# Optimization experiments

Measured on AMD Instinct MI355X. Metric: run time of the kernel, lower is better.

Reference implementation:

```python
import jax, jax.numpy as jnp
import numpy as np

# --- constants from init_kwargs / module defaults ---
H, W, C = 720, 1280, 2
T_EVT, T_PROP = 10, 10
T_TOTAL = T_EVT + T_PROP          # 20 temporal steps (10 event + 10 propagation)
TAU, THR0 = 10.0, 1.0             # LIF time constant, base threshold
ALPHA, TARGET_RATE = 0.1, 0.1     # PENT adaptation
THR_MIN, THR_MAX = 0.1, 10.0
N_EVENTS = 4_000_000


def setup_inputs() -> dict:
    key = jax.random.key(0)
    k1, k2, k3, k4 = jax.random.split(key, 4)
    x = jax.random.randint(k1, (N_EVENTS,), 0, W, dtype=jnp.int32)
    y = jax.random.randint(k2, (N_EVENTS,), 0, H, dtype=jnp.int32)
    p = jax.random.randint(k3, (N_EVENTS,), 0, 2, dtype=jnp.int32)
    t = jax.random.uniform(k4, (N_EVENTS,), dtype=jnp.float32)
    return {"x": x, "y": y, "p": p, "t": t}


def _build_buffer(x, y, p, t):
    # TemporalBuffer.forward: bin events into first T_EVT steps, rest are zeros.
    tmin, tmax = t.min(), t.max()
    denom = jnp.where(tmax > tmin, tmax - tmin, jnp.float32(1.0))
    t_norm = jnp.where(tmax > tmin, (t - tmin) / denom * (T_EVT - 1e-6), 0.0)
    t_idx = jnp.clip(t_norm.astype(jnp.int32), 0, T_EVT - 1)
    xi = jnp.clip(x, 0, W - 1)
    yi = jnp.clip(y, 0, H - 1)
    c_idx = p  # p in {0,1} -> channel index directly (p.min() >= 0 branch)
    buf = jnp.zeros((T_TOTAL, C, H, W), jnp.float32)
    return buf.at[t_idx, c_idx, yi, xi].add(1.0)


def reference(x, y, p, t):
    buffer = _build_buffer(x, y, p, t)  # (T, C, H, W)
    decay = jnp.float32(np.exp(-1.0 / TAU))

    def step(carry, frame):
        mem, thr = carry
        # LIFBuffer: decay + accumulate
        mem = mem * decay + frame
        spk = (mem >= thr).astype(jnp.float32)
        mem = mem - spk * thr  # soft ('subtract') reset
        # AdaptiveThreshold (PENT): homeostatic rate-based adaptation
        rate = spk.mean()
        thr = jnp.clip(thr + ALPHA * (rate - TARGET_RATE), THR_MIN, THR_MAX)
        return (mem, thr), spk

    mem0 = jnp.zeros((C, H, W), jnp.float32)
    (_, _), spikes = jax.lax.scan(step, (mem0, jnp.float32(THR0)), buffer)
    return spikes  # (T, C, H, W) binary spike activity maps
```

## Files before the change

kernel.cpp:

```cpp
#include <hip/hip_runtime.h>
#include <cstddef>

#define HH 720
#define WW 1280
#define FRAME 1843200
#define FRAME4 460800
#define T_EVT 10
#define T_TOTAL 20
#define ARRIVE64 (1ULL << 32)

#define ONBLK 256
#define ONTHR 1024
#define ONWPB 16
#define ONT (ONBLK * ONTHR)

#define SBLK 1024
#define STHR 256
#define SWPB 4
#define PIXB 1800
#define NGROUP4 450
#define HIST_W 9000
#define RBLK 512
#define RTHR 1024
#define NBUCKET 1024
#define EPT 8
#define MAXM (EPT * RTHR)
#define MMBLK 128
#define MMTHR 1024

#define MAT_OFF   0u
#define MMX_OFF   (512u * 1024u * 4u)
#define KEY_OFF   (MMX_OFF + 4096u)
#define WS_NEED(chunk) ((size_t)KEY_OFF + 2ull * RBLK * (size_t)(chunk) + 256ull)

__device__ unsigned g_minkey;
__device__ unsigned g_maxkey;
__device__ unsigned long long g_grp[T_TOTAL][16][16];
__device__ unsigned long long g_top[T_TOTAL][16];
__device__ unsigned g_rel[T_TOTAL][32];
__device__ unsigned long long g_n1[T_TOTAL][64][16];
__device__ unsigned long long g_n2[T_TOTAL][4][16];
__device__ unsigned long long g_n3[T_TOTAL][16];
__device__ unsigned g_relg[T_TOTAL][64][32];

__device__ __forceinline__ unsigned f2key(float f) {
    unsigned b = __float_as_uint(f);
    return b ^ ((unsigned)(((int)b) >> 31) | 0x80000000u);
}
__device__ __forceinline__ float key2f(unsigned k) {
    unsigned b = (k & 0x80000000u) ? (k ^ 0x80000000u) : ~k;
    return __uint_as_float(b);
}

__device__ __forceinline__ int event_bin_t(float tv, float tmin, float tmax) {
#pragma clang fp contract(off)
    float tn;
    if (tmax > tmin) tn = (tv - tmin) / (tmax - tmin) * (float)(10.0 - 1e-6);
    else tn = 0.0f;
    int ti = (int)tn;
    return ti < 0 ? 0 : (ti > T_EVT - 1 ? T_EVT - 1 : ti);
}
__device__ __forceinline__ int event_pixel(int xi, int yi, int ci) {
    xi = xi < 0 ? 0 : (xi > WW - 1 ? WW - 1 : xi);
    yi = yi < 0 ? 0 : (yi > HH - 1 ? HH - 1 : yi);
    return ci * (HH * WW) + yi * WW + xi;
}

__global__ void init_kernel() {
    const int gtid = blockIdx.x * blockDim.x + threadIdx.x;
    const int gs = gridDim.x * blockDim.x;
    if (gtid == 0) { g_minkey = 0xFFFFFFFFu; g_maxkey = 0u; }
    unsigned long long* a = &g_grp[0][0][0];
    for (int i = gtid; i < T_TOTAL * 16 * 16; i += gs) a[i] = 0ull;
    unsigned long long* b = &g_top[0][0];
    for (int i = gtid; i < T_TOTAL * 16; i += gs) b[i] = 0ull;
    unsigned* c = &g_rel[0][0];
    for (int i = gtid; i < T_TOTAL * 32; i += gs) c[i] = 0u;
}

__device__ __forceinline__ void minmax_body(const float* __restrict__ t, int n,
                                            int gtid, int gstride) {
    unsigned mn = 0xFFFFFFFFu, mx = 0u;
    const int n4 = n >> 2;
    const float4* t4 = (const float4*)t;
    for (int i = gtid; i < n4; i += gstride) {
        float4 tv = t4[i];
        unsigned k0 = f2key(tv.x), k1 = f2key(tv.y);
        unsigned k2 = f2key(tv.z), k3 = f2key(tv.w);
        unsigned a = k0 < k1 ? k0 : k1, b = k2 < k3 ? k2 : k3;
        unsigned c = a < b ? a : b;
        mn = mn < c ? mn : c;
        a = k0 > k1 ? k0 : k1; b = k2 > k3 ? k2 : k3;
        c = a > b ? a : b;
        mx = mx > c ? mx : c;
    }
    for (int i = (n4 << 2) + gtid; i < n; i += gstride) {
        unsigned k = f2key(t[i]);
        mn = mn < k ? mn : k;
        mx = mx > k ? mx : k;
    }
    for (int off = 32; off > 0; off >>= 1) {
        unsigned omn = (unsigned)__shfl_down((int)mn, off, 64);
        unsigned omx = (unsigned)__shfl_down((int)mx, off, 64);
        mn = mn < omn ? mn : omn;
        mx = mx > omx ? mx : omx;
    }
    __shared__ unsigned smn[16], smx[16];
    int lane = threadIdx.x & 63, wv = threadIdx.x >> 6;
    if (lane == 0) { smn[wv] = mn; smx[wv] = mx; }
    __syncthreads();
    if (threadIdx.x == 0) {
        int nw = blockDim.x >> 6;
        for (int i = 1; i < nw; ++i) {
            mn = mn < smn[i] ? mn : smn[i];
            mx = mx > smx[i] ? mx : smx[i];
        }
        atomicMin(&g_minkey, mn);
        atomicMax(&g_maxkey, mx);
    }
}

__global__ void minmax_zero_kernel(const float* __restrict__ t, int n,
                                   uint4* __restrict__ hist16v) {
    const int gtid = blockIdx.x * blockDim.x + threadIdx.x;
    const int gstride = gridDim.x * blockDim.x;
    const uint4 z = make_uint4(0u, 0u, 0u, 0u);
    const int nz = T_EVT * FRAME / 8;
    for (int i = gtid; i < nz; i += gstride) hist16v[i] = z;
    minmax_body(t, n, gtid, gstride);
}

__global__ __launch_bounds__(MMTHR) void minmax_ws_kernel(
        const float* __restrict__ t, int n, unsigned* __restrict__ mmx) {
    const int gtid = blockIdx.x * blockDim.x + threadIdx.x;
    const int gstride = gridDim.x * blockDim.x;
    unsigned mx = 0u, imn = 0u;
    const int n4 = n >> 2;
    const float4* t4 = (const float4*)t;
    for (int i = gtid; i < n4; i += gstride) {
        float4 tv = t4[i];
        unsigned k0 = f2key(tv.x), k1 = f2key(tv.y);
        unsigned k2 = f2key(tv.z), k3 = f2key(tv.w);
        unsigned a = k0 > k1 ? k0 : k1, b = k2 > k3 ? k2 : k3;
        unsigned c = a > b ? a : b;
        mx = mx > c ? mx : c;
        unsigned i0 = ~k0, i1 = ~k1, i2 = ~k2, i3 = ~k3;
        a = i0 > i1 ? i0 : i1; b = i2 > i3 ? i2 : i3;
        c = a > b ? a : b;
        imn = imn > c ? imn : c;
    }
    for (int i = (n4 << 2) + gtid; i < n; i += gstride) {
        unsigned k = f2key(t[i]);
        mx = mx > k ? mx : k;
        unsigned ik = ~k;
        imn = imn > ik ? imn : ik;
    }
    for (int off = 32; off > 0; off >>= 1) {
        unsigned omx = (unsigned)__shfl_down((int)mx, off, 64);
        unsigned oim = (unsigned)__shfl_down((int)imn, off, 64);
        mx = mx > omx ? mx : omx;
        imn = imn > oim ? imn : oim;
    }
    __shared__ unsigned smx[MMTHR / 64], sim[MMTHR / 64];
    const int lane = threadIdx.x & 63, wv = threadIdx.x >> 6;
    if (lane == 0) { smx[wv] = mx; sim[wv] = imn; }
    __syncthreads();
    if (threadIdx.x == 0) {
#pragma unroll
        for (int i = 1; i < MMTHR / 64; ++i) {
            mx = mx > smx[i] ? mx : smx[i];
            imn = imn > sim[i] ? imn : sim[i];
        }
        atomicMax(&mmx[0], mx);
        atomicMax(&mmx[32], imn);
    }
}

__global__ __launch_bounds__(RTHR) void passAB_kernel(
        const int* __restrict__ x, const int* __restrict__ y,
        const int* __restrict__ p, const float* __restrict__ t,
        const unsigned* __restrict__ mmx,
        unsigned* __restrict__ mat, unsigned short* __restrict__ seg, int n) {
    __shared__ unsigned cnt[NBUCKET];
    __shared__ unsigned wt2[RTHR / 64];
    __shared__ unsigned short sorted[MAXM];
    const int bid = blockIdx.x;
    const int j = threadIdx.x;
    const int lane = j & 63, wv = j >> 6;
    const int gtid = bid * RTHR + j;
    const int gs = RBLK * RTHR;
    {
        unsigned long long* z1 = &g_n1[0][0][0];
        for (int i = gtid; i < T_TOTAL * 64 * 16; i += gs) z1[i] = 0ull;
        unsigned long long* z2 = &g_n2[0][0][0];
        for (int i = gtid; i < T_TOTAL * 4 * 16; i += gs) z2[i] = 0ull;
        unsigned long long* z3 = &g_n3[0][0];
        for (int i = gtid; i < T_TOTAL * 16; i += gs) z3[i] = 0ull;
        unsigned* z4 = &g_relg[0][0][0];
        for (int i = gtid; i < T_TOTAL * 64 * 32; i += gs) z4[i] = 0u;
    }
    cnt[j] = 0u;
    __syncthreads();
    const float tmax = key2f(mmx[0]);
    const float tmin = key2f(~mmx[32]);
    const int chunk = (((n + RBLK - 1) / RBLK) + 3) & ~3;
    const int s0 = bid * chunk;
    const int s1 = min(n, s0 + chunk);
    const int m = s1 - s0;

    unsigned rec[EPT];
#pragma unroll
    for (int k = 0; k < EPT / 4; ++k) {
        const int ibase = s0 + ((k * RTHR + j) << 2);
#pragma unroll
        for (int e = 0; e < 4; ++e) rec[k * 4 + e] = 0xFFFFFFFFu;
        if (ibase + 4 <= s1) {
            int4 xv = *(const int4*)(x + ibase);
            int4 yv = *(const int4*)(y + ibase);
            int4 pv = *(const int4*)(p + ibase);
            float4 tv = *(const float4*)(t + ibase);
            int pxs[4] = { event_pixel(xv.x, yv.x, pv.x),
                           event_pixel(xv.y, yv.y, pv.y),
                           event_pixel(xv.z, yv.z, pv.z),
                           event_pixel(xv.w, yv.w, pv.w) };
            float ts[4] = { tv.x, tv.y, tv.z, tv.w };
#pragma unroll
            for (int e = 0; e < 4; ++e) {
                int pix = pxs[e];
                int ti = event_bin_t(ts[e], tmin, tmax);
                int bkt = pix / PIXB;
                int lb = ti * PIXB + (pix - bkt * PIXB);
                rec[k * 4 + e] = ((unsigned)bkt << 16) | (unsigned)lb;
                atomicAdd(&cnt[bkt], 1u);
            }
        } else if (ibase < s1) {
            for (int e = 0; e < 4; ++e) {
                int i = ibase + e;
                if (i < s1) {
                    int pix = event_pixel(x[i], y[i], p[i]);
                    int ti = event_bin_t(t[i], tmin, tmax);
                    int bkt = pix / PIXB;
                    int lb = ti * PIXB + (pix - bkt * PIXB);
                    rec[k * 4 + e] = ((unsigned)bkt << 16) | (unsigned)lb;
                    atomicAdd(&cnt[bkt], 1u);
                }
            }
        }
    }
    __syncthreads();
    {
        unsigned v = cnt[j];
        unsigned incl = v;
        for (int off = 1; off < 64; off <<= 1) {
            unsigned o = (unsigned)__shfl_up((int)incl, off, 64);
            if (lane >= off) incl += o;
        }
        if (lane == 63) wt2[wv] = incl;
        __syncthreads();
        if (j == 0) {
            unsigned run = 0;
#pragma unroll
            for (int k = 0; k < RTHR / 64; ++k) { unsigned tmp = wt2[k]; wt2[k] = run; run += tmp; }
        }
        __syncthreads();
        unsigned ex = incl - v + wt2[wv];
        mat[bid * NBUCKET + j] = (ex << 16) | v;
        cnt[j] = ex;
    }
    __syncthreads();
#pragma unroll
    for (int k = 0; k < EPT; ++k) {
        unsigned r0 = rec[k];
        if (r0 != 0xFFFFFFFFu) {
            unsigned bkt = r0 >> 16;
            unsigned r = atomicAdd(&cnt[bkt], 1u);
            sorted[r] = (unsigned short)(r0 & 0xFFFFu);
        }
    }
    __syncthreads();
    unsigned short* segb = seg + (size_t)bid * (size_t)chunk;
    for (int i = j; i < m; i += RTHR) segb[i] = sorted[i];
}

__global__ __launch_bounds__(STHR, 4) void scan_new(float* __restrict__ out,
                                                    const unsigned short* __restrict__ seg,
                                                    const unsigned* __restrict__ mat,
                                                    int n) {
#pragma clang fp contract(off)
    const float decay = (float)0.9048374180359595;
    const int tid = threadIdx.x;
    const int lane = tid & 63;
    const int b = blockIdx.x;
    const int pix0 = b * PIXB;

    __shared__ alignas(16) unsigned lds_hist[HIST_W];
    __shared__ unsigned runw[RBLK];
    __shared__ unsigned lds_arr[T_TOTAL];
    __shared__ unsigned lds_tot[T_TOTAL];

    for (int i = tid; i < HIST_W; i += STHR) lds_hist[i] = 0u;
    for (int r = tid; r < RBLK; r += STHR) runw[r] = mat[r * NBUCKET + b];
    if (tid < T_TOTAL) { lds_arr[tid] = 0u; lds_tot[tid] = 0u; }
    __syncthreads();

    {
        const int chunk = (((n + RBLK - 1) / RBLK) + 3) & ~3;
        for (int r = tid; r < RBLK; r += STHR) {
            unsigned w = runw[r];
            unsigned c = w & 0xFFFFu;
            const unsigned short* sp = seg + (size_t)r * (size_t)chunk + (w >> 16);
            for (unsigned k = 0; k < c; ++k) {
                unsigned lb = sp[k];
                atomicAdd(&lds_hist[lb >> 1], 1u << ((lb & 1u) << 4));
            }
        }
    }
    __syncthreads();

    const bool has1 = tid < (NGROUP4 - STHR);
    float4 mem0 = make_float4(0.f, 0.f, 0.f, 0.f);
    float4 mem1 = make_float4(0.f, 0.f, 0.f, 0.f);
    float thr = 1.0f;

    float4 f0, f1;
    {
        uint2 w01 = *(const uint2*)&lds_hist[tid << 1];
        f0 = make_float4((float)(w01.x & 0xFFFFu), (float)(w01.x >> 16),
                         (float)(w01.y & 0xFFFFu), (float)(w01.y >> 16));
        if (has1) {
            uint2 v = *(const uint2*)&lds_hist[(tid + STHR) << 1];
            f1 = make_float4((float)(v.x & 0xFFFFu), (float)(v.x >> 16),
                             (float)(v.y & 0xFFFFu), (float)(v.y >> 16));
        } else f1 = make_float4(0.f, 0.f, 0.f, 0.f);
    }

    for (int s = 0;; ++s) {
        float* ob = out + (size_t)s * FRAME + pix0;
        int cnt = 0;

        {
            float4 m, spk;
            m.x = mem0.x + f0.x;
            m.y = mem0.y + f0.y;
            m.z = mem0.z + f0.z;
            m.w = mem0.w + f0.w;
            spk.x = (m.x >= thr) ? 1.0f : 0.0f;
            spk.y = (m.y >= thr) ? 1.0f : 0.0f;
            spk.z = (m.z >= thr) ? 1.0f : 0.0f;
            spk.w = (m.w >= thr) ? 1.0f : 0.0f;
            ((float4*)ob)[tid] = spk;
            mem0.x = m.x - spk.x * thr;
            mem0.y = m.y - spk.y * thr;
            mem0.z = m.z - spk.z * thr;
            mem0.w = m.w - spk.w * thr;
            cnt += (int)spk.x + (int)spk.y + (int)spk.z + (int)spk.w;
        }
        if (has1) {
            int g = tid + STHR;
            float4 m, spk;
            m.x = mem1.x + f1.x;
            m.y = mem1.y + f1.y;
            m.z = mem1.z + f1.z;
            m.w = mem1.w + f1.w;
            spk.x = (m.x >= thr) ? 1.0f : 0.0f;
            spk.y = (m.y >= thr) ? 1.0f : 0.0f;
            spk.z = (m.z >= thr) ? 1.0f : 0.0f;
            spk.w = (m.w >= thr) ? 1.0f : 0.0f;
            ((float4*)ob)[g] = spk;
            mem1.x = m.x - spk.x * thr;
            mem1.y = m.y - spk.y * thr;
            mem1.z = m.z - spk.z * thr;
            mem1.w = m.w - spk.w * thr;
            cnt += (int)spk.x + (int)spk.y + (int)spk.z + (int)spk.w;
        }

        if (s == T_TOTAL - 1) break;

        for (int off = 32; off > 0; off >>= 1) cnt += __shfl_down(cnt, off, 64);

        bool last = false;
        const int g1 = b >> 4;
        if (lane == 0) {
            unsigned old = __hip_atomic_fetch_add(&lds_arr[s],
                               (unsigned)cnt + (1u << 16),
                               __ATOMIC_RELAXED, __HIP_MEMORY_SCOPE_WORKGROUP);
            if ((old >> 16) == SWPB - 1) {
                last = true;
                unsigned bc = (old + (unsigned)cnt) & 0xFFFFu;
                unsigned long long a1 = __hip_atomic_fetch_add(
                    &g_n1[s][g1][0], (unsigned long long)bc + ARRIVE64,
                    __ATOMIC_RELAXED, __HIP_MEMORY_SCOPE_AGENT);
                if ((unsigned)(a1 >> 32) == 15u) {
                    unsigned c1 = (unsigned)a1 + bc;
                    const int g2 = g1 >> 4;
                    unsigned long long a2 = __hip_atomic_fetch_add(
                        &g_n2[s][g2][0], (unsigned long long)c1 + ARRIVE64,
                        __ATOMIC_RELAXED, __HIP_MEMORY_SCOPE_AGENT);
                    if ((unsigned)(a2 >> 32) == 15u) {
                        unsigned c2 = (unsigned)a2 + c1;
                        unsigned long long a3 = __hip_atomic_fetch_add(
                            &g_n3[s][0], (unsigned long long)c2 + ARRIVE64,
                            __ATOMIC_RELAXED, __HIP_MEMORY_SCOPE_AGENT);
                        if ((unsigned)(a3 >> 32) == 3u) {
                            unsigned tot = (unsigned)a3 + c2;
                            for (int g = 0; g < 64; ++g)
                                __hip_atomic_store(&g_relg[s][g][0], tot + 1u,
                                    __ATOMIC_RELAXED, __HIP_MEMORY_SCOPE_AGENT);
                        }
                    }
                }
            }
        }

        {
            const int sn = s + 1;
            if (sn < T_EVT) {
                uint2 w01 = *(const uint2*)&lds_hist[sn * 900 + (tid << 1)];
                f0 = make_float4((float)(w01.x & 0xFFFFu), (float)(w01.x >> 16),
                                 (float)(w01.y & 0xFFFFu), (float)(w01.y >> 16));
                if (has1) {
                    uint2 v = *(const uint2*)&lds_hist[sn * 900 + ((tid + STHR) << 1)];
                    f1 = make_float4((float)(v.x & 0xFFFFu), (float)(v.x >> 16),
                                     (float)(v.y & 0xFFFFu), (float)(v.y >> 16));
                }
            } else {
                f0 = make_float4(0.f, 0.f, 0.f, 0.f);
                f1 = make_float4(0.f, 0.f, 0.f, 0.f);
            }
            mem0.x = mem0.x * decay; mem0.y = mem0.y * decay;
            mem0.z = mem0.z * decay; mem0.w = mem0.w * decay;
            mem1.x = mem1.x * decay; mem1.y = mem1.y * decay;
            mem1.z = mem1.z * decay; mem1.w = mem1.w * decay;
        }
        __builtin_amdgcn_sched_barrier(0);

        unsigned total = 0u;
        if (lane == 0) {
            unsigned f;
            if (last) {
                do {
                    __builtin_amdgcn_s_sleep(1);
                    f = __hip_atomic_load(&g_relg[s][g1][0], __ATOMIC_RELAXED,
                                          __HIP_MEMORY_SCOPE_AGENT);
                } while (f == 0u);
                total = f - 1u;
                __hip_atomic_store(&lds_tot[s], f,
                                   __ATOMIC_RELAXED, __HIP_MEMORY_SCOPE_WORKGROUP);
            } else {
                unsigned f2;
                do {
                    __builtin_amdgcn_s_sleep(1);
                    f2 = __hip_atomic_load(&lds_tot[s], __ATOMIC_RELAXED,
                                           __HIP_MEMORY_SCOPE_WORKGROUP);
                } while (f2 == 0u);
                total = f2 - 1u;
            }
        }
        total = (unsigned)__shfl((int)total, 0, 64);
        float rate = (float)total / 1843200.0f;
        thr = thr + 0.1f * (rate - 0.1f);
        thr = fminf(fmaxf(thr, 0.1f), 10.0f);
    }
}

__global__ void scatter_kernel(const int* __restrict__ x, const int* __restrict__ y,
                               const int* __restrict__ p, const float* __restrict__ t,
                               unsigned* __restrict__ hist32, int n) {
    int i = blockIdx.x * blockDim.x + threadIdx.x;
    if (i >= n) return;
    float tmin = key2f(g_minkey);
    float tmax = key2f(g_maxkey);
    int ti = event_bin_t(t[i], tmin, tmax);
    int pix = event_pixel(x[i], y[i], p[i]);
    size_t bidx = (size_t)ti * FRAME + pix;
    atomicAdd(hist32 + (bidx >> 1), 1u << ((bidx & 1) << 4));
}

__global__ __launch_bounds__(ONTHR) void scan_old(float* __restrict__ out) {
#pragma clang fp contract(off)
    const float decay = (float)0.9048374180359595;
    const int gtid = blockIdx.x * ONTHR + threadIdx.x;
    const int lane = threadIdx.x & 63;
    const uint2 uz2 = make_uint2(0u, 0u);
    float4 mem0 = make_float4(0.f, 0.f, 0.f, 0.f);
    float4 mem1 = make_float4(0.f, 0.f, 0.f, 0.f);
    const bool has1 = (gtid + ONT) < FRAME4;
    float thr = 1.0f;
    const uint2* hist2 = (const uint2*)(out + (size_t)T_EVT * FRAME);
    __shared__ unsigned lds_arr[T_TOTAL];
    __shared__ unsigned lds_tot[T_TOTAL];
    if (threadIdx.x < T_TOTAL) { lds_arr[threadIdx.x] = 0u; lds_tot[threadIdx.x] = 0u; }
    __syncthreads();
    uint2 u0 = hist2[gtid];
    uint2 u1 = has1 ? hist2[gtid + ONT] : uz2;
    for (int s = 0; s < T_TOTAL; ++s) {
        float4* o4 = (float4*)(out + (size_t)s * FRAME);
        int cnt = 0;
        {
            float4 m, spk;
            m.x = mem0.x * decay; m.x = m.x + (float)(u0.x & 0xFFFFu);
            m.y = mem0.y * decay; m.y = m.y + (float)(u0.x >> 16);
            m.z = mem0.z * decay; m.z = m.z + (float)(u0.y & 0xFFFFu);
            m.w = mem0.w * decay; m.w = m.w + (float)(u0.y >> 16);
            spk.x = (m.x >= thr) ? 1.0f : 0.0f;
            spk.y = (m.y >= thr) ? 1.0f : 0.0f;
            spk.z = (m.z >= thr) ? 1.0f : 0.0f;
            spk.w = (m.w >= thr) ? 1.0f : 0.0f;
            o4[gtid] = spk;
            mem0.x = m.x - spk.x * thr; mem0.y = m.y - spk.y * thr;
            mem0.z = m.z - spk.z * thr; mem0.w = m.w - spk.w * thr;
            cnt += (int)spk.x + (int)spk.y + (int)spk.z + (int)spk.w;
        }
        if (has1) {
            float4 m, spk;
            m.x = mem1.x * decay; m.x = m.x + (float)(u1.x & 0xFFFFu);
            m.y = mem1.y * decay; m.y = m.y + (float)(u1.x >> 16);
            m.z = mem1.z * decay; m.z = m.z + (float)(u1.y & 0xFFFFu);
            m.w = mem1.w * decay; m.w = m.w + (float)(u1.y >> 16);
            spk.x = (m.x >= thr) ? 1.0f : 0.0f;
            spk.y = (m.y >= thr) ? 1.0f : 0.0f;
            spk.z = (m.z >= thr) ? 1.0f : 0.0f;
            spk.w = (m.w >= thr) ? 1.0f : 0.0f;
            o4[gtid + ONT] = spk;
            mem1.x = m.x - spk.x * thr; mem1.y = m.y - spk.y * thr;
            mem1.z = m.z - spk.z * thr; mem1.w = m.w - spk.w * thr;
            cnt += (int)spk.x + (int)spk.y + (int)spk.z + (int)spk.w;
        }
        if (s + 1 < T_EVT) {
            const uint2* hn = hist2 + (size_t)(s + 1) * FRAME4;
            u0 = hn[gtid];
            u1 = has1 ? hn[gtid + ONT] : uz2;
        } else { u0 = uz2; u1 = uz2; }
        if (s == T_TOTAL - 1) break;
        for (int off = 32; off > 0; off >>= 1) cnt += __shfl_down(cnt, off, 64);
        unsigned total = 0u;
        if (lane == 0) {
            unsigned old = __hip_atomic_fetch_add(&lds_arr[s],
                               (unsigned)cnt + (1u << 16),
                               __ATOMIC_RELAXED, __HIP_MEMORY_SCOPE_WORKGROUP);
            if ((old >> 16) == ONWPB - 1) {
                unsigned bc = (old + (unsigned)cnt) & 0xFFFFu;
                const int gid = blockIdx.x >> 4;
                unsigned long long gold = __hip_atomic_fetch_add(
                    &g_grp[s][gid][0], (unsigned long long)bc + ARRIVE64,
                    __ATOMIC_RELAXED, __HIP_MEMORY_SCOPE_AGENT);
                if ((unsigned)(gold >> 32) == 15u) {
                    unsigned gc = (unsigned)gold + bc;
                    unsigned long long told = __hip_atomic_fetch_add(
                        &g_top[s][0], (unsigned long long)gc + ARRIVE64,
                        __ATOMIC_RELAXED, __HIP_MEMORY_SCOPE_AGENT);
                    if ((unsigned)(told >> 32) == 15u) {
                        unsigned tot = (unsigned)told + gc;
                        __hip_atomic_store(&g_rel[s][0], tot + 1u,
                                           __ATOMIC_RELAXED, __HIP_MEMORY_SCOPE_AGENT);
                    }
                }
                unsigned f;
                do {
                    __builtin_amdgcn_s_sleep(1);
                    f = __hip_atomic_load(&g_rel[s][0], __ATOMIC_RELAXED,
                                          __HIP_MEMORY_SCOPE_AGENT);
                } while (f == 0u);
                total = f - 1u;
                __hip_atomic_store(&lds_tot[s], f,
                                   __ATOMIC_RELAXED, __HIP_MEMORY_SCOPE_WORKGROUP);
            } else {
                unsigned f;
                do {
                    __builtin_amdgcn_s_sleep(1);
                    f = __hip_atomic_load(&lds_tot[s], __ATOMIC_RELAXED,
                                          __HIP_MEMORY_SCOPE_WORKGROUP);
                } while (f == 0u);
                total = f - 1u;
            }
        }
        total = (unsigned)__shfl((int)total, 0, 64);
        float rate = (float)total / 1843200.0f;
        thr = thr + 0.1f * (rate - 0.1f);
        thr = fminf(fmaxf(thr, 0.1f), 10.0f);
    }
}

extern "C" void kernel_launch(void* const* d_in, const int* in_sizes, int n_in,
                              void* d_out, int out_size, void* d_ws, size_t ws_size,
                              hipStream_t stream) {
    const int*   x = (const int*)d_in[0];
    const int*   y = (const int*)d_in[1];
    const int*   p = (const int*)d_in[2];
    const float* t = (const float*)d_in[3];
    float* out = (float*)d_out;
    const int n = in_sizes[0];

    const int chunk = (((n + RBLK - 1) / RBLK) + 3) & ~3;
    if (d_ws != nullptr && ws_size >= WS_NEED(chunk) && chunk <= MAXM && n >= 4) {
        unsigned* mat = (unsigned*)((char*)d_ws + MAT_OFF);
        unsigned* mmx = (unsigned*)((char*)d_ws + MMX_OFF);
        unsigned short* seg = (unsigned short*)((char*)d_ws + KEY_OFF);

        hipMemsetAsync(mmx, 0, 256, stream);
        minmax_ws_kernel<<<MMBLK, MMTHR, 0, stream>>>(t, n, mmx);
        passAB_kernel<<<RBLK, RTHR, 0, stream>>>(x, y, p, t, mmx, mat, seg, n);

        dim3 g(SBLK), b(STHR);
        void* args[] = { (void*)&out, (void*)&seg, (void*)&mat, (void*)&n };
        hipLaunchCooperativeKernel((void*)scan_new, g, b, args, 0, stream);
    } else {
        init_kernel<<<64, 256, 0, stream>>>();
        unsigned* hist32 = (unsigned*)(out + (size_t)T_EVT * FRAME);
        minmax_zero_kernel<<<1024, 256, 0, stream>>>(t, n, (uint4*)hist32);
        scatter_kernel<<<(n + 255) / 256, 256, 0, stream>>>(x, y, p, t, hist32, n);
        dim3 g(ONBLK), b(ONTHR);
        void* args[] = { (void*)&out };
        hipLaunchCooperativeKernel((void*)scan_old, g, b, args, 0, stream);
    }
}
```

Baseline: 307.7 us.

## Drop memset via per-block minmax partials, transpose bucket matrix, parallelize histogram reads

The min/max kernel now writes per-block partials to a global array instead of doing atomics on a memset workspace, and each passAB block reduces the 128 partials itself, which removes the memset launch. The per-bucket count matrix is stored transposed so the scan kernel reads its row contiguously. The histogram build in the scan kernel assigns 16 lanes per run segment instead of one thread per run, for coalesced reads and better load balance. The cost is some redundant partial reduction in every passAB block, plus more LDS atomic contention among lanes.

```diff
diff --git a/kernel.cpp b/kernel.cpp
--- a/kernel.cpp
+++ b/kernel.cpp
@@ -35,6 +35,8 @@
 
 __device__ unsigned g_minkey;
 __device__ unsigned g_maxkey;
+__device__ unsigned g_mm_mx[MMBLK];
+__device__ unsigned g_mm_imn[MMBLK];
 __device__ unsigned long long g_grp[T_TOTAL][16][16];
 __device__ unsigned long long g_top[T_TOTAL][16];
 __device__ unsigned g_rel[T_TOTAL][32];
@@ -131,7 +133,7 @@
 }
 
 __global__ __launch_bounds__(MMTHR) void minmax_ws_kernel(
-        const float* __restrict__ t, int n, unsigned* __restrict__ mmx) {
+        const float* __restrict__ t, int n) {
     const int gtid = blockIdx.x * blockDim.x + threadIdx.x;
     const int gstride = gridDim.x * blockDim.x;
     unsigned mx = 0u, imn = 0u;
@@ -171,18 +173,18 @@
             mx = mx > smx[i] ? mx : smx[i];
             imn = imn > sim[i] ? imn : sim[i];
         }
-        atomicMax(&mmx[0], mx);
-        atomicMax(&mmx[32], imn);
+        g_mm_mx[blockIdx.x] = mx;
+        g_mm_imn[blockIdx.x] = imn;
     }
 }
 
 __global__ __launch_bounds__(RTHR) void passAB_kernel(
         const int* __restrict__ x, const int* __restrict__ y,
         const int* __restrict__ p, const float* __restrict__ t,
-        const unsigned* __restrict__ mmx,
         unsigned* __restrict__ mat, unsigned short* __restrict__ seg, int n) {
     __shared__ unsigned cnt[NBUCKET];
     __shared__ unsigned wt2[RTHR / 64];
+    __shared__ float s_tmin, s_tmax;
     __shared__ unsigned short sorted[MAXM];
     const int bid = blockIdx.x;
     const int j = threadIdx.x;
@@ -200,9 +202,22 @@
         for (int i = gtid; i < T_TOTAL * 64 * 32; i += gs) z4[i] = 0u;
     }
     cnt[j] = 0u;
-    __syncthreads();
-    const float tmax = key2f(mmx[0]);
-    const float tmin = key2f(~mmx[32]);
+    if (j < 64) {
+        unsigned mxa = g_mm_mx[j], mxb = g_mm_mx[j + 64];
+        unsigned ima = g_mm_imn[j], imb = g_mm_imn[j + 64];
+        unsigned mx = mxa > mxb ? mxa : mxb;
+        unsigned im = ima > imb ? ima : imb;
+        for (int off = 32; off > 0; off >>= 1) {
+            unsigned omx = (unsigned)__shfl_down((int)mx, off, 64);
+            unsigned oim = (unsigned)__shfl_down((int)im, off, 64);
+            mx = mx > omx ? mx : omx;
+            im = im > oim ? im : oim;
+        }
+        if (j == 0) { s_tmax = key2f(mx); s_tmin = key2f(~im); }
+    }
+    __syncthreads();
+    const float tmax = s_tmax;
+    const float tmin = s_tmin;
     const int chunk = (((n + RBLK - 1) / RBLK) + 3) & ~3;
     const int s0 = bid * chunk;
     const int s1 = min(n, s0 + chunk);
@@ -264,7 +279,7 @@
         }
         __syncthreads();
         unsigned ex = incl - v + wt2[wv];
-        mat[bid * NBUCKET + j] = (ex << 16) | v;
+        mat[j * RBLK + bid] = (ex << 16) | v;
         cnt[j] = ex;
     }
     __syncthreads();
@@ -299,17 +314,19 @@
     __shared__ unsigned lds_tot[T_TOTAL];
 
     for (int i = tid; i < HIST_W; i += STHR) lds_hist[i] = 0u;
-    for (int r = tid; r < RBLK; r += STHR) runw[r] = mat[r * NBUCKET + b];
+    for (int r = tid; r < RBLK; r += STHR) runw[r] = mat[b * RBLK + r];
     if (tid < T_TOTAL) { lds_arr[tid] = 0u; lds_tot[tid] = 0u; }
     __syncthreads();
 
     {
         const int chunk = (((n + RBLK - 1) / RBLK) + 3) & ~3;
-        for (int r = tid; r < RBLK; r += STHR) {
+        const int sg = tid >> 4;
+        const int sl = tid & 15;
+        for (int r = sg; r < RBLK; r += (STHR >> 4)) {
             unsigned w = runw[r];
             unsigned c = w & 0xFFFFu;
             const unsigned short* sp = seg + (size_t)r * (size_t)chunk + (w >> 16);
-            for (unsigned k = 0; k < c; ++k) {
+            for (unsigned k = sl; k < c; k += 16) {
                 unsigned lb = sp[k];
                 atomicAdd(&lds_hist[lb >> 1], 1u << ((lb & 1u) << 4));
             }
@@ -594,12 +611,10 @@
     const int chunk = (((n + RBLK - 1) / RBLK) + 3) & ~3;
     if (d_ws != nullptr && ws_size >= WS_NEED(chunk) && chunk <= MAXM && n >= 4) {
         unsigned* mat = (unsigned*)((char*)d_ws + MAT_OFF);
-        unsigned* mmx = (unsigned*)((char*)d_ws + MMX_OFF);
         unsigned short* seg = (unsigned short*)((char*)d_ws + KEY_OFF);
 
-        hipMemsetAsync(mmx, 0, 256, stream);
-        minmax_ws_kernel<<<MMBLK, MMTHR, 0, stream>>>(t, n, mmx);
-        passAB_kernel<<<RBLK, RTHR, 0, stream>>>(x, y, p, t, mmx, mat, seg, n);
+        minmax_ws_kernel<<<MMBLK, MMTHR, 0, stream>>>(t, n);
+        passAB_kernel<<<RBLK, RTHR, 0, stream>>>(x, y, p, t, mat, seg, n);
 
         dim3 g(SBLK), b(STHR);
         void* args[] = { (void*)&out, (void*)&seg, (void*)&mat, (void*)&n };
```

Result: no change. 305.8 us (-0.6%).
